# Kernel tuning notes

Hardware: AMD Instinct MI355X
Metric: run time of the kernel (lower is better)

The kernel has to match this reference:

```python
import jax, jax.numpy as jnp
import numpy as np

N = 8192        # n_nodes
NFEAT = 512
NHID = 256
AVG_DEG = 32
K = 64          # mean_kwargs k
TEMP = 1.0      # mean_kwargs temperature


def setup_inputs() -> dict:
    key = jax.random.key(0)
    ks = jax.random.split(key, 5)
    x = jax.random.normal(ks[0], (N, NFEAT), jnp.float32)
    edge_index = jax.random.randint(ks[1], (2, N * AVG_DEG), 0, N, dtype=jnp.int64)
    W1 = jax.random.normal(ks[2], (NFEAT, NHID), jnp.float32) / np.sqrt(NFEAT)
    b1 = jnp.zeros((NHID,), jnp.float32)
    W2 = jax.random.normal(ks[3], (NHID, NHID), jnp.float32) / np.sqrt(NHID)
    b2 = jnp.zeros((NHID,), jnp.float32)
    return {"x": x, "edge_index": edge_index, "W1": W1, "b1": b1, "W2": W2, "b2": b2}


def _gcn_norm(edge_index, n, dtype):
    # PyG gcn_norm: add self-loops (weight 1), deg over col, sym normalization
    loops = jnp.arange(n, dtype=edge_index.dtype)
    row = jnp.concatenate([edge_index[0], loops])
    col = jnp.concatenate([edge_index[1], loops])
    w = jnp.ones(row.shape[0], dtype)
    deg = jnp.zeros((n,), dtype).at[col].add(w)
    dis = jnp.where(deg > 0, jax.lax.rsqrt(jnp.where(deg > 0, deg, 1.0)), 0.0)
    return row, col, dis[row] * w * dis[col]


def _soft_k_medoid(row, col, w, x):
    # soft_weighted_medoid_k_neighborhood(A, x, k=K, temperature=TEMP, with_weight_correction=True)
    n, d = x.shape
    A = jnp.zeros((n, n), x.dtype).at[row, col].add(w)   # coalesced dense adjacency
    topk_a, topk_idx = jax.lax.top_k(A, K)               # [n, K] neighbor weights / ids
    xk = x[topk_idx]                                     # [n, K, d]
    sq = jnp.sum(xk * xk, axis=-1)                       # [n, K]
    G = jnp.einsum('nkd,nld->nkl', xk, xk)               # Gram per node
    d2 = jnp.maximum(sq[:, :, None] + sq[:, None, :] - 2.0 * G, 0.0)
    pos = d2 > 0
    dist = jnp.where(pos, jnp.sqrt(jnp.where(pos, d2, 1.0)), 0.0)  # safe sqrt (grad-safe)
    # weighted sum of distances to each top-k candidate j: c[n,j] = sum_l a[n,l] * ||x_l - x_j||
    c = jnp.einsum('nl,nlj->nj', topk_a, dist)
    c = jnp.where(topk_a == 0, jnp.finfo(x.dtype).max, c)
    soft = jax.nn.softmax(-c / TEMP, axis=-1)            # [n, K]
    soft = soft * topk_a                                 # with_weight_correction
    soft = soft / jnp.sum(soft, axis=-1, keepdims=True)
    row_sum = jnp.sum(A, axis=-1)                        # preserve neighborhood mass
    return row_sum[:, None] * jnp.einsum('nk,nkd->nd', soft, xk)


def reference(x, edge_index, W1, b1, W2, b2):
    n = x.shape[0]
    row, col, w = _gcn_norm(edge_index, n, x.dtype)
    h = jax.nn.relu(_soft_k_medoid(row, col, w, x @ W1) + b1)   # gc1 + relu (dropout: eval = identity)
    return jax.nn.relu(_soft_k_medoid(row, col, w, h @ W2) + b2)  # gc2 + relu
```

## Files before the change

### kernel.cpp

```cpp
#include <hip/hip_runtime.h>

typedef _Float16 half4 __attribute__((ext_vector_type(4)));
typedef _Float16 half8 __attribute__((ext_vector_type(8)));
typedef float f32x4 __attribute__((ext_vector_type(4)));

#define NNODE 8192
#define NHID  256
#define RCAP  128
#define KCAP  64
#define GLS   72
#define SK    136

struct SmemGemm { _Float16 sA[64][GLS]; _Float16 sB[64][GLS]; };

struct DedupScratch {
    int lc[RCAP]; float lw[RCAP]; unsigned char kp[RCAP];
    int cw[2]; float rw[2];
};

struct SmemMedoid {
    union { _Float16 sh[64][SK]; DedupScratch dd; } u;
    float s_a[64]; float s_sq[64]; float s_cpart[2][64]; float s_u[64];
    int s_cols[64]; float s_red[4][288]; float s_rsum;
};

__device__ __forceinline__ void gemm_body(
    char* smraw, const float* __restrict__ Af32, const _Float16* __restrict__ Ahi,
    const float* __restrict__ W, _Float16* __restrict__ Chi,
    int K, int af32, int bm, int bn) {
    SmemGemm& sm = *(SmemGemm*)smraw;
    const int t = threadIdx.x;
    const int lane = t & 63, L15 = lane & 15, q = lane >> 4;
    const int w = t >> 6, wr = w >> 1, wc = w & 1;
    f32x4 acc[2][2];
#pragma unroll
    for (int a = 0; a < 2; ++a)
#pragma unroll
        for (int b2 = 0; b2 < 2; ++b2) acc[a][b2] = (f32x4){0.f, 0.f, 0.f, 0.f};

    for (int k0 = 0; k0 < K; k0 += 64) {
        if (af32) {
#pragma unroll
            for (int i = 0; i < 4; ++i) {
                int row = i * 16 + (t >> 4), kc = (t & 15) * 4;
                float4 v = *(const float4*)(Af32 + (size_t)(bm + row) * K + k0 + kc);
                half4 h;
                h[0] = (_Float16)v.x; h[1] = (_Float16)v.y;
                h[2] = (_Float16)v.z; h[3] = (_Float16)v.w;
                *(half4*)&sm.sA[row][kc] = h;
            }
        } else {
#pragma unroll
            for (int i = 0; i < 2; ++i) {
                int row = i * 32 + (t >> 3), ch = t & 7;
                *(half8*)&sm.sA[row][ch * 8] =
                    *(const half8*)(Ahi + (size_t)(bm + row) * K + k0 + ch * 8);
            }
        }
#pragma unroll
        for (int i = 0; i < 4; ++i) {
            int krow = i * 16 + (t >> 4), nc4 = (t & 15) * 4;
            float4 v = *(const float4*)(W + (size_t)(k0 + krow) * NHID + bn + nc4);
            sm.sB[nc4 + 0][krow] = (_Float16)v.x;
            sm.sB[nc4 + 1][krow] = (_Float16)v.y;
            sm.sB[nc4 + 2][krow] = (_Float16)v.z;
            sm.sB[nc4 + 3][krow] = (_Float16)v.w;
        }
        __syncthreads();
#pragma unroll
        for (int ks = 0; ks < 2; ++ks) {
            const int ko = ks * 32 + q * 8;
            half8 ah[2], bh[2];
#pragma unroll
            for (int tr = 0; tr < 2; ++tr)
                ah[tr] = *(const half8*)&sm.sA[32 * wr + 16 * tr + L15][ko];
#pragma unroll
            for (int tc = 0; tc < 2; ++tc)
                bh[tc] = *(const half8*)&sm.sB[32 * wc + 16 * tc + L15][ko];
#pragma unroll
            for (int tr = 0; tr < 2; ++tr)
#pragma unroll
                for (int tc = 0; tc < 2; ++tc)
                    acc[tr][tc] = __builtin_amdgcn_mfma_f32_16x16x32_f16(ah[tr], bh[tc], acc[tr][tc], 0, 0, 0);
        }
        __syncthreads();
    }
#pragma unroll
    for (int tr = 0; tr < 2; ++tr)
#pragma unroll
        for (int tc = 0; tc < 2; ++tc)
#pragma unroll
            for (int r = 0; r < 4; ++r) {
                int rowg = bm + 32 * wr + 16 * tr + q * 4 + r;
                int colg = bn + 32 * wc + 16 * tc + L15;
                Chi[(size_t)rowg * NHID + colg] = (_Float16)acc[tr][tc][r];
            }
}

__device__ __forceinline__ void medoid_core(
    SmemMedoid& sm, const _Float16* __restrict__ Xhi, const float* __restrict__ bias,
    float* __restrict__ OutF, _Float16* __restrict__ OutHi, int node, int writeH) {
    const int t = threadIdx.x;
    const int w = t >> 6, lane = t & 63;
    const int L15 = lane & 15, q = lane >> 4;
    const int wr = w >> 1, wc = w & 1;

    f32x4 acc[2][2];
#pragma unroll
    for (int a = 0; a < 2; ++a)
#pragma unroll
        for (int b = 0; b < 2; ++b) acc[a][b] = (f32x4){0.f, 0.f, 0.f, 0.f};

    const int ch = t & 15, rr = t >> 4;
    for (int phase = 0; phase < 2; ++phase) {
#pragma unroll
        for (int i = 0; i < 4; ++i) {
            int l = i * 16 + rr;
            *(half8*)&sm.u.sh[l][ch * 8] =
                *(const half8*)(Xhi + ((size_t)sm.s_cols[l] << 8) + phase * 128 + ch * 8);
        }
        __syncthreads();
#pragma unroll
        for (int ks = 0; ks < 4; ++ks) {
            const int ko = ks * 32 + q * 8;
            half8 ah[2], bh[2];
#pragma unroll
            for (int tr = 0; tr < 2; ++tr) ah[tr] = *(const half8*)&sm.u.sh[32 * wr + 16 * tr + L15][ko];
#pragma unroll
            for (int tc = 0; tc < 2; ++tc) bh[tc] = *(const half8*)&sm.u.sh[32 * wc + 16 * tc + L15][ko];
#pragma unroll
            for (int tr = 0; tr < 2; ++tr)
#pragma unroll
                for (int tc = 0; tc < 2; ++tc)
                    acc[tr][tc] = __builtin_amdgcn_mfma_f32_16x16x32_f16(ah[tr], bh[tc], acc[tr][tc], 0, 0, 0);
        }
        if (phase == 0) __syncthreads();
    }

#pragma unroll
    for (int tr = 0; tr < 2; ++tr)
#pragma unroll
        for (int tc = 0; tc < 2; ++tc)
            if (32 * wr + 16 * tr == 32 * wc + 16 * tc) {
#pragma unroll
                for (int r = 0; r < 4; ++r)
                    if (L15 == q * 4 + r) sm.s_sq[32 * wr + 16 * tr + L15] = acc[tr][tc][r];
            }
    __syncthreads();

    f32x4 sq4[2], a4[2];
#pragma unroll
    for (int tr = 0; tr < 2; ++tr) {
        sq4[tr] = *(const f32x4*)&sm.s_sq[32 * wr + 16 * tr + 4 * q];
        a4[tr]  = *(const f32x4*)&sm.s_a [32 * wr + 16 * tr + 4 * q];
    }
#pragma unroll
    for (int tc = 0; tc < 2; ++tc) {
        const int colg = 32 * wc + 16 * tc + L15;
        const float sqc = sm.s_sq[colg];
        float pj = 0.f;
#pragma unroll
        for (int tr = 0; tr < 2; ++tr)
#pragma unroll
            for (int r = 0; r < 4; ++r) {
                float d2 = sq4[tr][r] + sqc - 2.f * acc[tr][tc][r];
                float dist = d2 > 0.f ? __builtin_amdgcn_sqrtf(d2) : 0.f;
                pj = fmaf(a4[tr][r], dist, pj);
            }
        pj += __shfl_xor(pj, 16, 64);
        pj += __shfl_xor(pj, 32, 64);
        if (q == 0) sm.s_cpart[wr][colg] = pj;
    }
    __syncthreads();

    if (w == 0) {
        int j = lane;
        float c = sm.s_cpart[0][j] + sm.s_cpart[1][j];
        float aj = sm.s_a[j];
        bool valid = aj > 0.f;
        float cv = valid ? c : 3.4e38f;
        float mn = cv;
#pragma unroll
        for (int d = 1; d < 64; d <<= 1) mn = fminf(mn, __shfl_xor(mn, d, 64));
        float e = valid ? __expf(mn - c) * aj : 0.f;
        float s = e;
#pragma unroll
        for (int d = 1; d < 64; d <<= 1) s += __shfl_xor(s, d, 64);
        sm.s_u[j] = e * (sm.s_rsum / s);
    }
    __syncthreads();

    const int oct = t & 31, jb = t >> 5;
    float accd[8] = {0.f, 0.f, 0.f, 0.f, 0.f, 0.f, 0.f, 0.f};
#pragma unroll
    for (int jj = 0; jj < 8; ++jj) {
        int j = jb * 8 + jj;
        float u = sm.s_u[j];
        half8 xv;
        if (oct < 16) xv = *(const half8*)(Xhi + ((size_t)sm.s_cols[j] << 8) + oct * 8);
        else          xv = *(const half8*)&sm.u.sh[j][(oct - 16) * 8];
#pragma unroll
        for (int e = 0; e < 8; ++e) accd[e] = fmaf(u, (float)xv[e], accd[e]);
    }
#pragma unroll
    for (int e = 0; e < 8; ++e) accd[e] += __shfl_xor(accd[e], 32, 64);
    if (lane < 32) {
#pragma unroll
        for (int e = 0; e < 8; ++e) sm.s_red[w][9 * oct + e] = accd[e];
    }
    __syncthreads();
    const int idx = 9 * (t >> 3) + (t & 7);
    float o = sm.s_red[0][idx] + sm.s_red[1][idx] + sm.s_red[2][idx] + sm.s_red[3][idx];
    float res = fmaxf(o + bias[t], 0.f);
    size_t oi = (size_t)node * NHID + t;
    if (writeH) OutHi[oi] = (_Float16)res;
    else        OutF[oi] = res;
}

__global__ __launch_bounds__(256) void k_s1(
    const float* __restrict__ x, const float* __restrict__ W1, const void* edges,
    int* rowcnt, int* nbr, int* deg, int E, _Float16* __restrict__ X1) {
    if ((int)blockIdx.x < 512) {
        __shared__ __align__(16) char smem[sizeof(SmemGemm)];
        int g = blockIdx.x;
        gemm_body(smem, x, nullptr, W1, X1, 512, 1, (g >> 2) * 64, (g & 3) * 64);
    } else {
        __shared__ int sflag;
        const int t = threadIdx.x;
        if (t < 64) {
            const long long* e = (const long long*)edges;
            long long v = e[t];
            unsigned long long bad = __ballot(v < 0 || v >= (long long)NNODE);
            if (t == 0) sflag = (bad == 0) ? 1 : 0;
        }
        __syncthreads();
        const int fl = sflag;
        int i = ((int)blockIdx.x - 512) * 256 + t;
        if (i >= E + NNODE) return;
        int r, c;
        if (i < E) {
            if (fl) {
                const long long* e = (const long long*)edges;
                r = (int)e[i]; c = (int)e[E + i];
            } else {
                const int* e = (const int*)edges;
                r = e[i]; c = e[E + i];
            }
        } else { r = i - E; c = r; }
        int pos = atomicAdd(&rowcnt[r], 1);
        if (pos < RCAP) nbr[r * RCAP + pos] = c;
        atomicAdd(&deg[c], 1);
    }
}

__global__ __launch_bounds__(256, 6) void k_medoid1(
    const _Float16* __restrict__ X, const float* __restrict__ b1,
    _Float16* __restrict__ Hh,
    const int* __restrict__ nbr, const int* __restrict__ rowcnt,
    const int* __restrict__ deg,
    int* __restrict__ cols, float* __restrict__ wA, float* __restrict__ rsum) {
    __shared__ __align__(16) SmemMedoid sm;
    const int r = blockIdx.x, t = threadIdx.x;
    const int w = t >> 6, lane = t & 63;

    int n = rowcnt[r]; if (n > RCAP) n = RCAP;
    if (t < n) sm.u.dd.lc[t] = nbr[r * RCAP + t];
    __syncthreads();
    float dr = 1.f / sqrtf((float)deg[r]);
    bool keep = false; float wv = 0.f; int myc = 0;
    if (t < n) {
        myc = sm.u.dd.lc[t];
        int mult = 0; bool first = true;
        for (int i = 0; i < n; ++i) {
            int ci = sm.u.dd.lc[i];
            if (ci == myc) { mult++; if (i < t) first = false; }
        }
        keep = first;
        if (first) wv = (float)mult * dr * (1.f / sqrtf((float)deg[myc]));
    }
    if (t < RCAP) { sm.u.dd.kp[t] = keep ? 1 : 0; sm.u.dd.lw[t] = wv; }
    int pre = 0;
    if (w < 2) {
        float rv = wv;
#pragma unroll
        for (int d = 1; d < 64; d <<= 1) rv += __shfl_xor(rv, d, 64);
        unsigned long long b = __ballot(keep);
        pre = __popcll(b & ((1ull << lane) - 1ull));
        int cw = __popcll(b);
        if (lane == 0) { sm.u.dd.cw[w] = cw; sm.u.dd.rw[w] = rv; }
    }
    __syncthreads();
    int total = sm.u.dd.cw[0] + sm.u.dd.cw[1];
    float rs = sm.u.dd.rw[0] + sm.u.dd.rw[1];
    if (t == 0) { rsum[r] = rs; sm.s_rsum = rs; }
    const int base = r * KCAP;
    if (total <= KCAP) {
        if (w < 2 && keep) {
            int off = (w ? sm.u.dd.cw[0] : 0) + pre;
            cols[base + off] = myc; wA[base + off] = wv;
            sm.s_cols[off] = myc;   sm.s_a[off] = wv;
        }
        for (int m = total + t; m < KCAP; m += 256) {
            cols[base + m] = r; wA[base + m] = 0.f;
            sm.s_cols[m] = r;   sm.s_a[m] = 0.f;
        }
    } else if (t == 0) {
        for (int s = 0; s < KCAP; ++s) {
            int best = -1;
            for (int i = 0; i < n; ++i) {
                if (!sm.u.dd.kp[i]) continue;
                if (best < 0 || sm.u.dd.lw[i] > sm.u.dd.lw[best] ||
                    (sm.u.dd.lw[i] == sm.u.dd.lw[best] && sm.u.dd.lc[i] < sm.u.dd.lc[best])) best = i;
            }
            cols[base + s] = sm.u.dd.lc[best]; wA[base + s] = sm.u.dd.lw[best];
            sm.s_cols[s] = sm.u.dd.lc[best];   sm.s_a[s] = sm.u.dd.lw[best];
            sm.u.dd.kp[best] = 0;
        }
    }
    __syncthreads();

    medoid_core(sm, X, b1, nullptr, Hh, r, 1);
}

__global__ __launch_bounds__(256) void k_gemm2(
    const _Float16* __restrict__ Hh, const float* __restrict__ W2,
    _Float16* __restrict__ X2) {
    __shared__ __align__(16) char smem[sizeof(SmemGemm)];
    gemm_body(smem, nullptr, Hh, W2, X2, 256, 0, blockIdx.x * 64, blockIdx.y * 64);
}

__global__ __launch_bounds__(256, 6) void k_medoid2(
    const _Float16* __restrict__ X, const float* __restrict__ b2,
    float* __restrict__ out,
    const int* __restrict__ cols, const float* __restrict__ wts,
    const float* __restrict__ rsum) {
    __shared__ __align__(16) SmemMedoid sm;
    const int node = blockIdx.x, t = threadIdx.x;
    if (t < 64) { sm.s_cols[t] = cols[node * KCAP + t]; sm.s_a[t] = wts[node * KCAP + t]; }
    if (t == 0) sm.s_rsum = rsum[node];
    __syncthreads();
    medoid_core(sm, X, b2, out, nullptr, node, 0);
}

extern "C" void kernel_launch(void* const* d_in, const int* in_sizes, int n_in,
                              void* d_out, int out_size, void* d_ws, size_t ws_size,
                              hipStream_t stream) {
    const float* x  = (const float*)d_in[0];
    const void*  ei = d_in[1];
    const float* W1 = (const float*)d_in[2];
    const float* b1 = (const float*)d_in[3];
    const float* W2 = (const float*)d_in[4];
    const float* b2 = (const float*)d_in[5];
    float* out = (float*)d_out;
    const int E = in_sizes[1] / 2;

    char* p = (char*)d_ws;
    auto alloc = [&](size_t bytes) { char* q = p; p += (bytes + 255) & ~(size_t)255; return q; };
    int*      cnt   = (int*)alloc((size_t)2 * NNODE * 4);
    int*      deg    = cnt;
    int*      rowcnt = cnt + NNODE;
    int*      colsA  = (int*)alloc((size_t)NNODE * KCAP * 4);
    float*    wAr    = (float*)alloc((size_t)NNODE * KCAP * 4);
    float*    rsum   = (float*)alloc((size_t)NNODE * 4);
    _Float16* X1     = (_Float16*)alloc((size_t)NNODE * NHID * 2);
    _Float16* Hh     = (_Float16*)alloc((size_t)NNODE * NHID * 2);
    int*      nbr    = (int*)alloc((size_t)NNODE * RCAP * 4);

    const int nscat = (E + NNODE + 255) / 256;

    hipMemsetAsync(cnt, 0, (size_t)2 * NNODE * 4, stream);
    k_s1<<<512 + nscat, 256, 0, stream>>>(x, W1, ei, rowcnt, nbr, deg, E, X1);
    k_medoid1<<<NNODE, 256, 0, stream>>>(X1, b1, Hh, nbr, rowcnt, deg, colsA, wAr, rsum);
    k_gemm2<<<dim3(NNODE / 64, NHID / 64), 256, 0, stream>>>(Hh, W2, X1);
    k_medoid2<<<NNODE, 256, 0, stream>>>(X1, b2, out, colsA, wAr, rsum);
}
```

Before: 220.7 us.

## Pre-convert inputs to fp16, fuse dedup into GEMM1 launch, unify medoid kernels

Adds a prep kernel that converts x to fp16 and stores W1/W2 transposed in fp16, so the GEMM loads fp16 tiles directly without in-loop conversion or scattered transposed stores. Neighbor dedup/top-k selection is moved out of the first medoid kernel into the GEMM1 launch as separate blocks handling two rows each, so the medoid kernels become a single shared implementation. This trades an extra full pass over x through memory for simpler GEMM inner loops and better overlap of dedup with GEMM work.

```diff
diff --git a/kernel.cpp b/kernel.cpp
--- a/kernel.cpp
+++ b/kernel.cpp
@@ -11,23 +11,18 @@
 #define GLS   72
 #define SK    136
 
-struct SmemGemm { _Float16 sA[64][GLS]; _Float16 sB[64][GLS]; };
-
-struct DedupScratch {
-    int lc[RCAP]; float lw[RCAP]; unsigned char kp[RCAP];
-    int cw[2]; float rw[2];
-};
-
+struct SmemGemm  { _Float16 sA[64][GLS]; _Float16 sB[64][GLS]; };
+struct SmemDedup { int lc[2][RCAP]; float lw[2][RCAP]; unsigned char kp[2][RCAP];
+                   int cw[2][2]; float rw[2][2]; };
 struct SmemMedoid {
-    union { _Float16 sh[64][SK]; DedupScratch dd; } u;
+    _Float16 sh[64][SK];
     float s_a[64]; float s_sq[64]; float s_cpart[2][64]; float s_u[64];
     int s_cols[64]; float s_red[4][288]; float s_rsum;
 };
 
 __device__ __forceinline__ void gemm_body(
-    char* smraw, const float* __restrict__ Af32, const _Float16* __restrict__ Ahi,
-    const float* __restrict__ W, _Float16* __restrict__ Chi,
-    int K, int af32, int bm, int bn) {
+    char* smraw, const _Float16* __restrict__ Ahi, const _Float16* __restrict__ BT,
+    _Float16* __restrict__ Chi, int K, int bm, int bn) {
     SmemGemm& sm = *(SmemGemm*)smraw;
     const int t = threadIdx.x;
     const int lane = t & 63, L15 = lane & 15, q = lane >> 4;
@@ -39,32 +34,13 @@
         for (int b2 = 0; b2 < 2; ++b2) acc[a][b2] = (f32x4){0.f, 0.f, 0.f, 0.f};
 
     for (int k0 = 0; k0 < K; k0 += 64) {
-        if (af32) {
-#pragma unroll
-            for (int i = 0; i < 4; ++i) {
-                int row = i * 16 + (t >> 4), kc = (t & 15) * 4;
-                float4 v = *(const float4*)(Af32 + (size_t)(bm + row) * K + k0 + kc);
-                half4 h;
-                h[0] = (_Float16)v.x; h[1] = (_Float16)v.y;
-                h[2] = (_Float16)v.z; h[3] = (_Float16)v.w;
-                *(half4*)&sm.sA[row][kc] = h;
-            }
-        } else {
-#pragma unroll
-            for (int i = 0; i < 2; ++i) {
-                int row = i * 32 + (t >> 3), ch = t & 7;
-                *(half8*)&sm.sA[row][ch * 8] =
-                    *(const half8*)(Ahi + (size_t)(bm + row) * K + k0 + ch * 8);
-            }
-        }
-#pragma unroll
-        for (int i = 0; i < 4; ++i) {
-            int krow = i * 16 + (t >> 4), nc4 = (t & 15) * 4;
-            float4 v = *(const float4*)(W + (size_t)(k0 + krow) * NHID + bn + nc4);
-            sm.sB[nc4 + 0][krow] = (_Float16)v.x;
-            sm.sB[nc4 + 1][krow] = (_Float16)v.y;
-            sm.sB[nc4 + 2][krow] = (_Float16)v.z;
-            sm.sB[nc4 + 3][krow] = (_Float16)v.w;
+#pragma unroll
+        for (int i = 0; i < 2; ++i) {
+            int row = i * 32 + (t >> 3), ch = t & 7;
+            *(half8*)&sm.sA[row][ch * 8] =
+                *(const half8*)(Ahi + (size_t)(bm + row) * K + k0 + ch * 8);
+            *(half8*)&sm.sB[row][ch * 8] =
+                *(const half8*)(BT + (size_t)(bn + row) * K + k0 + ch * 8);
         }
         __syncthreads();
 #pragma unroll
@@ -95,6 +71,59 @@
                 int colg = bn + 32 * wc + 16 * tc + L15;
                 Chi[(size_t)rowg * NHID + colg] = (_Float16)acc[tr][tc][r];
             }
+}
+
+__device__ __forceinline__ void dedup_body(
+    char* smraw, const int* __restrict__ nbr, const int* __restrict__ rowcnt,
+    const int* __restrict__ deg, int* __restrict__ cols, float* __restrict__ wout,
+    float* __restrict__ rsum, int grp) {
+    SmemDedup& sm = *(SmemDedup*)smraw;
+    const int t = threadIdx.x;
+    const int half = t >> 7, st = t & 127;
+    const int wid = st >> 6, lane = t & 63;
+    const int r = grp * 2 + half;
+    int n = rowcnt[r]; if (n > RCAP) n = RCAP;
+    if (st < n) sm.lc[half][st] = nbr[r * RCAP + st];
+    __syncthreads();
+    float dr = 1.f / sqrtf((float)deg[r]);
+    bool keep = false; float wv = 0.f;
+    if (st < n) {
+        int c = sm.lc[half][st];
+        int mult = 0; bool first = true;
+        for (int i = 0; i < n; ++i) {
+            int ci = sm.lc[half][i];
+            if (ci == c) { mult++; if (i < st) first = false; }
+        }
+        keep = first;
+        if (first) wv = (float)mult * dr * (1.f / sqrtf((float)deg[c]));
+    }
+    sm.kp[half][st] = keep ? 1 : 0; sm.lw[half][st] = wv;
+    float rv = wv;
+#pragma unroll
+    for (int d = 1; d < 64; d <<= 1) rv += __shfl_xor(rv, d, 64);
+    unsigned long long b = __ballot(keep);
+    int pre = __popcll(b & ((1ull << lane) - 1ull));
+    int cw = __popcll(b);
+    if (lane == 0) { sm.cw[half][wid] = cw; sm.rw[half][wid] = rv; }
+    __syncthreads();
+    int total = sm.cw[half][0] + sm.cw[half][1];
+    if (st == 0) rsum[r] = sm.rw[half][0] + sm.rw[half][1];
+    const int base = r * KCAP;
+    if (total <= KCAP) {
+        int off = (wid ? sm.cw[half][0] : 0) + pre;
+        if (keep) { cols[base + off] = sm.lc[half][st]; wout[base + off] = wv; }
+        for (int m = total + st; m < KCAP; m += 128) { cols[base + m] = r; wout[base + m] = 0.f; }
+    } else if (st == 0) {
+        for (int s = 0; s < KCAP; ++s) {
+            int best = -1;
+            for (int i = 0; i < n; ++i) {
+                if (!sm.kp[half][i]) continue;
+                if (best < 0 || sm.lw[half][i] > sm.lw[half][best] ||
+                    (sm.lw[half][i] == sm.lw[half][best] && sm.lc[half][i] < sm.lc[half][best])) best = i;
+            }
+            cols[base + s] = sm.lc[half][best]; wout[base + s] = sm.lw[half][best]; sm.kp[half][best] = 0;
+        }
+    }
 }
 
 __device__ __forceinline__ void medoid_core(
@@ -116,7 +145,7 @@
 #pragma unroll
         for (int i = 0; i < 4; ++i) {
             int l = i * 16 + rr;
-            *(half8*)&sm.u.sh[l][ch * 8] =
+            *(half8*)&sm.sh[l][ch * 8] =
                 *(const half8*)(Xhi + ((size_t)sm.s_cols[l] << 8) + phase * 128 + ch * 8);
         }
         __syncthreads();
@@ -125,9 +154,9 @@
             const int ko = ks * 32 + q * 8;
             half8 ah[2], bh[2];
 #pragma unroll
-            for (int tr = 0; tr < 2; ++tr) ah[tr] = *(const half8*)&sm.u.sh[32 * wr + 16 * tr + L15][ko];
-#pragma unroll
-            for (int tc = 0; tc < 2; ++tc) bh[tc] = *(const half8*)&sm.u.sh[32 * wc + 16 * tc + L15][ko];
+            for (int tr = 0; tr < 2; ++tr) ah[tr] = *(const half8*)&sm.sh[32 * wr + 16 * tr + L15][ko];
+#pragma unroll
+            for (int tc = 0; tc < 2; ++tc) bh[tc] = *(const half8*)&sm.sh[32 * wc + 16 * tc + L15][ko];
 #pragma unroll
             for (int tr = 0; tr < 2; ++tr)
 #pragma unroll
@@ -198,7 +227,7 @@
         float u = sm.s_u[j];
         half8 xv;
         if (oct < 16) xv = *(const half8*)(Xhi + ((size_t)sm.s_cols[j] << 8) + oct * 8);
-        else          xv = *(const half8*)&sm.u.sh[j][(oct - 16) * 8];
+        else          xv = *(const half8*)&sm.sh[j][(oct - 16) * 8];
 #pragma unroll
         for (int e = 0; e < 8; ++e) accd[e] = fmaf(u, (float)xv[e], accd[e]);
     }
@@ -217,16 +246,32 @@
     else        OutF[oi] = res;
 }
 
-__global__ __launch_bounds__(256) void k_s1(
-    const float* __restrict__ x, const float* __restrict__ W1, const void* edges,
-    int* rowcnt, int* nbr, int* deg, int E, _Float16* __restrict__ X1) {
-    if ((int)blockIdx.x < 512) {
-        __shared__ __align__(16) char smem[sizeof(SmemGemm)];
-        int g = blockIdx.x;
-        gemm_body(smem, x, nullptr, W1, X1, 512, 1, (g >> 2) * 64, (g & 3) * 64);
+#define PREPB 512
+__global__ __launch_bounds__(256) void k_prep_scatter(
+    const float* __restrict__ x, _Float16* __restrict__ xh,
+    const float* __restrict__ W1, _Float16* __restrict__ w1T,
+    const float* __restrict__ W2, _Float16* __restrict__ w2T,
+    const void* edges, int* rowcnt, int* nbr, int* deg, int E) {
+    const int t = threadIdx.x;
+    if ((int)blockIdx.x < PREPB) {
+        const int gid = blockIdx.x * 256 + t, nthr = PREPB * 256;
+        for (int i = gid; i < NNODE * 512 / 4; i += nthr) {
+            float4 v = ((const float4*)x)[i];
+            half4 h;
+            h[0] = (_Float16)v.x; h[1] = (_Float16)v.y;
+            h[2] = (_Float16)v.z; h[3] = (_Float16)v.w;
+            *(half4*)&xh[4 * (size_t)i] = h;
+        }
+        for (int i = gid; i < 512 * NHID; i += nthr) {
+            int k = i >> 8, n = i & 255;
+            w1T[(size_t)n * 512 + k] = (_Float16)W1[i];
+        }
+        for (int i = gid; i < NHID * NHID; i += nthr) {
+            int k = i >> 8, n = i & 255;
+            w2T[(size_t)n * 256 + k] = (_Float16)W2[i];
+        }
     } else {
         __shared__ int sflag;
-        const int t = threadIdx.x;
         if (t < 64) {
             const long long* e = (const long long*)edges;
             long long v = e[t];
@@ -235,7 +280,7 @@
         }
         __syncthreads();
         const int fl = sflag;
-        int i = ((int)blockIdx.x - 512) * 256 + t;
+        int i = ((int)blockIdx.x - PREPB) * 256 + t;
         if (i >= E + NNODE) return;
         int r, c;
         if (i < E) {
@@ -253,93 +298,39 @@
     }
 }
 
-__global__ __launch_bounds__(256, 6) void k_medoid1(
-    const _Float16* __restrict__ X, const float* __restrict__ b1,
-    _Float16* __restrict__ Hh,
+__global__ __launch_bounds__(256) void k_gemm1_dedup(
+    const _Float16* __restrict__ xh, const _Float16* __restrict__ w1T,
+    _Float16* __restrict__ X1,
     const int* __restrict__ nbr, const int* __restrict__ rowcnt,
     const int* __restrict__ deg,
     int* __restrict__ cols, float* __restrict__ wA, float* __restrict__ rsum) {
-    __shared__ __align__(16) SmemMedoid sm;
-    const int r = blockIdx.x, t = threadIdx.x;
-    const int w = t >> 6, lane = t & 63;
-
-    int n = rowcnt[r]; if (n > RCAP) n = RCAP;
-    if (t < n) sm.u.dd.lc[t] = nbr[r * RCAP + t];
-    __syncthreads();
-    float dr = 1.f / sqrtf((float)deg[r]);
-    bool keep = false; float wv = 0.f; int myc = 0;
-    if (t < n) {
-        myc = sm.u.dd.lc[t];
-        int mult = 0; bool first = true;
-        for (int i = 0; i < n; ++i) {
-            int ci = sm.u.dd.lc[i];
-            if (ci == myc) { mult++; if (i < t) first = false; }
-        }
-        keep = first;
-        if (first) wv = (float)mult * dr * (1.f / sqrtf((float)deg[myc]));
-    }
-    if (t < RCAP) { sm.u.dd.kp[t] = keep ? 1 : 0; sm.u.dd.lw[t] = wv; }
-    int pre = 0;
-    if (w < 2) {
-        float rv = wv;
-#pragma unroll
-        for (int d = 1; d < 64; d <<= 1) rv += __shfl_xor(rv, d, 64);
-        unsigned long long b = __ballot(keep);
-        pre = __popcll(b & ((1ull << lane) - 1ull));
-        int cw = __popcll(b);
-        if (lane == 0) { sm.u.dd.cw[w] = cw; sm.u.dd.rw[w] = rv; }
-    }
-    __syncthreads();
-    int total = sm.u.dd.cw[0] + sm.u.dd.cw[1];
-    float rs = sm.u.dd.rw[0] + sm.u.dd.rw[1];
-    if (t == 0) { rsum[r] = rs; sm.s_rsum = rs; }
-    const int base = r * KCAP;
-    if (total <= KCAP) {
-        if (w < 2 && keep) {
-            int off = (w ? sm.u.dd.cw[0] : 0) + pre;
-            cols[base + off] = myc; wA[base + off] = wv;
-            sm.s_cols[off] = myc;   sm.s_a[off] = wv;
-        }
-        for (int m = total + t; m < KCAP; m += 256) {
-            cols[base + m] = r; wA[base + m] = 0.f;
-            sm.s_cols[m] = r;   sm.s_a[m] = 0.f;
-        }
-    } else if (t == 0) {
-        for (int s = 0; s < KCAP; ++s) {
-            int best = -1;
-            for (int i = 0; i < n; ++i) {
-                if (!sm.u.dd.kp[i]) continue;
-                if (best < 0 || sm.u.dd.lw[i] > sm.u.dd.lw[best] ||
-                    (sm.u.dd.lw[i] == sm.u.dd.lw[best] && sm.u.dd.lc[i] < sm.u.dd.lc[best])) best = i;
-            }
-            cols[base + s] = sm.u.dd.lc[best]; wA[base + s] = sm.u.dd.lw[best];
-            sm.s_cols[s] = sm.u.dd.lc[best];   sm.s_a[s] = sm.u.dd.lw[best];
-            sm.u.dd.kp[best] = 0;
-        }
-    }
-    __syncthreads();
-
-    medoid_core(sm, X, b1, nullptr, Hh, r, 1);
-}
-
-__global__ __launch_bounds__(256) void k_gemm2(
-    const _Float16* __restrict__ Hh, const float* __restrict__ W2,
-    _Float16* __restrict__ X2) {
     __shared__ __align__(16) char smem[sizeof(SmemGemm)];
-    gemm_body(smem, nullptr, Hh, W2, X2, 256, 0, blockIdx.x * 64, blockIdx.y * 64);
-}
-
-__global__ __launch_bounds__(256, 6) void k_medoid2(
-    const _Float16* __restrict__ X, const float* __restrict__ b2,
-    float* __restrict__ out,
+    if ((int)blockIdx.x < 512) {
+        int g = blockIdx.x;
+        gemm_body(smem, xh, w1T, X1, 512, (g >> 2) * 64, (g & 3) * 64);
+    } else {
+        dedup_body(smem, nbr, rowcnt, deg, cols, wA, rsum, (int)blockIdx.x - 512);
+    }
+}
+
+__global__ __launch_bounds__(256, 6) void k_medoid(
+    const _Float16* __restrict__ X, const float* __restrict__ bias,
+    float* __restrict__ OutF, _Float16* __restrict__ OutHi,
     const int* __restrict__ cols, const float* __restrict__ wts,
-    const float* __restrict__ rsum) {
+    const float* __restrict__ rsum, int writeH) {
     __shared__ __align__(16) SmemMedoid sm;
     const int node = blockIdx.x, t = threadIdx.x;
     if (t < 64) { sm.s_cols[t] = cols[node * KCAP + t]; sm.s_a[t] = wts[node * KCAP + t]; }
     if (t == 0) sm.s_rsum = rsum[node];
     __syncthreads();
-    medoid_core(sm, X, b2, out, nullptr, node, 0);
+    medoid_core(sm, X, bias, OutF, OutHi, node, writeH);
+}
+
+__global__ __launch_bounds__(256) void k_gemm2(
+    const _Float16* __restrict__ Hh, const _Float16* __restrict__ w2T,
+    _Float16* __restrict__ X2) {
+    __shared__ __align__(16) char smem[sizeof(SmemGemm)];
+    gemm_body(smem, Hh, w2T, X2, 256, blockIdx.x * 64, blockIdx.y * 64);
 }
 
 extern "C" void kernel_launch(void* const* d_in, const int* in_sizes, int n_in,
@@ -356,12 +347,15 @@
 
     char* p = (char*)d_ws;
     auto alloc = [&](size_t bytes) { char* q = p; p += (bytes + 255) & ~(size_t)255; return q; };
-    int*      cnt   = (int*)alloc((size_t)2 * NNODE * 4);
+    int*      cnt    = (int*)alloc((size_t)2 * NNODE * 4);
     int*      deg    = cnt;
     int*      rowcnt = cnt + NNODE;
     int*      colsA  = (int*)alloc((size_t)NNODE * KCAP * 4);
     float*    wAr    = (float*)alloc((size_t)NNODE * KCAP * 4);
     float*    rsum   = (float*)alloc((size_t)NNODE * 4);
+    _Float16* xh     = (_Float16*)alloc((size_t)NNODE * 512 * 2);
+    _Float16* w1T    = (_Float16*)alloc((size_t)512 * NHID * 2);
+    _Float16* w2T    = (_Float16*)alloc((size_t)NHID * NHID * 2);
     _Float16* X1     = (_Float16*)alloc((size_t)NNODE * NHID * 2);
     _Float16* Hh     = (_Float16*)alloc((size_t)NNODE * NHID * 2);
     int*      nbr    = (int*)alloc((size_t)NNODE * RCAP * 4);
@@ -369,8 +363,11 @@
     const int nscat = (E + NNODE + 255) / 256;
 
     hipMemsetAsync(cnt, 0, (size_t)2 * NNODE * 4, stream);
-    k_s1<<<512 + nscat, 256, 0, stream>>>(x, W1, ei, rowcnt, nbr, deg, E, X1);
-    k_medoid1<<<NNODE, 256, 0, stream>>>(X1, b1, Hh, nbr, rowcnt, deg, colsA, wAr, rsum);
-    k_gemm2<<<dim3(NNODE / 64, NHID / 64), 256, 0, stream>>>(Hh, W2, X1);
-    k_medoid2<<<NNODE, 256, 0, stream>>>(X1, b2, out, colsA, wAr, rsum);
-}
+    k_prep_scatter<<<PREPB + nscat, 256, 0, stream>>>(x, xh, W1, w1T, W2, w2T,
+                                                      ei, rowcnt, nbr, deg, E);
+    k_gemm1_dedup<<<512 + NNODE / 2, 256, 0, stream>>>(xh, w1T, X1, nbr, rowcnt, deg,
+                                                       colsA, wAr, rsum);
+    k_medoid<<<NNODE, 256, 0, stream>>>(X1, b1, nullptr, Hh, colsA, wAr, rsum, 1);
+    k_gemm2<<<dim3(NNODE / 64, NHID / 64), 256, 0, stream>>>(Hh, w2T, X1);
+    k_medoid<<<NNODE, 256, 0, stream>>>(X1, b2, out, nullptr, colsA, wAr, rsum, 0);
+}
```

Measured after the change: 213.1 us. 3.4% less time.
